# Optimization experiments

Hardware: AMD Instinct MI355X
Metric: run time of the kernel (lower is better)

The kernel has to match this reference:

```python
import jax, jax.numpy as jnp
import numpy as np

N, E, EMB, H, DH, FF, L = 2500, 10000, 32, 4, 8, 32, 1
EPS = 1e-5


def setup_inputs() -> dict:
    key = jax.random.key(0)
    ks = jax.random.split(key, 20)
    rn = lambda k, shape, s=0.1: jax.random.normal(k, shape, jnp.float32) * s
    return {
        'feat': rn(ks[0], (N, EMB), 1.0),
        'query': rn(ks[1], (E, L, H, DH)),
        'src_key_w': rn(ks[2], (E, L, H, FF, EMB)),
        'dst_key_w': rn(ks[3], (E, L, H, FF, EMB)),
        'src_key_b': rn(ks[4], (E, L, H, FF)),
        'dst_key_b': rn(ks[5], (E, L, H, FF)),
        'edge_key_w': rn(ks[6], (E, L, H, FF, DH)),
        'edge_key_b': rn(ks[7], (E, L, H, DH)),
        'src_val_w': rn(ks[8], (E, L, H, FF, EMB)),
        'dst_val_w': rn(ks[9], (E, L, H, FF, EMB)),
        'src_val_b': rn(ks[10], (E, L, H, FF)),
        'dst_val_b': rn(ks[11], (E, L, H, FF)),
        'edge_val_w': rn(ks[12], (E, L, H, FF, DH)),
        'edge_val_b': rn(ks[13], (E, L, H, DH)),
        'key_gamma': jnp.ones((DH,), jnp.float32),
        'key_beta': jnp.zeros((DH,), jnp.float32),
        'val_gamma': jnp.ones((DH,), jnp.float32),
        'val_beta': jnp.zeros((DH,), jnp.float32),
        'out_gamma': jnp.ones((DH,), jnp.float32),
        'out_beta': jnp.zeros((DH,), jnp.float32),
        'src': jax.random.randint(ks[14], (E,), 0, N, jnp.int32),
        'dst': jax.random.randint(ks[15], (E,), 0, N, jnp.int32),
        'i': 0,
    }


def _ln(x, g, b):
    m = x.mean(-1, keepdims=True)
    v = x.var(-1, keepdims=True)
    return (x - m) * jax.lax.rsqrt(v + EPS) * g + b


def _ffn(fs, fd, uw, vw, ub, vb, ew, eb, g, b):
    # per-edge, per-head two-layer feedforward with distinct weights
    # fs, fd: (E, EMB); uw/vw: (E,H,FF,EMB); ew: (E,H,FF,DH)
    h = (jnp.einsum('ehfd,ed->ehf', uw, fs) + ub
         + jnp.einsum('ehfd,ed->ehf', vw, fd) + vb)
    h = jax.nn.relu(h)
    o = jnp.einsum('ehfk,ehf->ehk', ew, h) + eb  # (E,H,DH)
    return _ln(o, g, b)


def reference(feat, query, src_key_w, dst_key_w, src_key_b, dst_key_b,
              edge_key_w, edge_key_b, src_val_w, dst_val_w, src_val_b,
              dst_val_b, edge_val_w, edge_val_b, key_gamma, key_beta,
              val_gamma, val_beta, out_gamma, out_beta, src, dst, i):
    n = feat.shape[0]
    fs, fd = feat[src], feat[dst]
    k = _ffn(fs, fd, src_key_w[:, i], dst_key_w[:, i], src_key_b[:, i],
             dst_key_b[:, i], edge_key_w[:, i], edge_key_b[:, i],
             key_gamma, key_beta)
    logits = (k * query[:, i]).sum(-1)  # (E,H)
    # edge softmax grouped by destination node
    m = jax.ops.segment_max(logits, dst, num_segments=n)
    ex = jnp.exp(logits - m[dst])
    s = jax.ops.segment_sum(ex, dst, num_segments=n)
    attn = ex / s[dst]  # (E,H)
    v = _ffn(fs, fd, src_val_w[:, i], dst_val_w[:, i], src_val_b[:, i],
             dst_val_b[:, i], edge_val_w[:, i], edge_val_b[:, i],
             val_gamma, val_beta)
    msg = v * attn[..., None]  # (E,H,DH)
    agg = jax.ops.segment_sum(msg, dst, num_segments=n)  # (N,H,DH)
    out = _ln(agg, out_gamma, out_beta)
    return out.reshape(feat.shape), attn
```

## Files before the change

kernel.cpp:

```cpp
#include <hip/hip_runtime.h>

#define NN   2500
#define NE   10000
#define EMBD 32
#define NH   4
#define DHD  8
#define FFD  32
#define EPSC 1e-5f

typedef float vf4 __attribute__((ext_vector_type(4)));

__device__ __forceinline__ float dot4v(vf4 a, vf4 b) {
    return a.x * b.x + a.y * b.y + a.z * b.z + a.w * b.w;
}

__device__ __forceinline__ vf4 ffn_compute(
    const vf4* U, const vf4* V, vf4 E, vf4 FS, vf4 FD,
    float b1, vf4 b2, vf4 g4, vf4 bt4, int lane)
{
    float p0 = dot4v(U[0], FS) + dot4v(V[0], FD);
    float p1 = dot4v(U[1], FS) + dot4v(V[1], FD);
    float p2 = dot4v(U[2], FS) + dot4v(V[2], FD);
    float p3 = dot4v(U[3], FS) + dot4v(V[3], FD);
    #pragma unroll
    for (int m = 1; m <= 4; m <<= 1) {
        p0 += __shfl_xor(p0, m); p1 += __shfl_xor(p1, m);
        p2 += __shfl_xor(p2, m); p3 += __shfl_xor(p3, m);
    }

    int f = lane >> 1;
    int s = ((f & 7) << 3) | (lane & 7);
    float h0 = __shfl(p0, s), h1 = __shfl(p1, s);
    float h2 = __shfl(p2, s), h3 = __shfl(p3, s);
    int j = lane >> 4;
    float hp = (j == 0) ? h0 : (j == 1) ? h1 : (j == 2) ? h2 : h3;
    float h  = fmaxf(hp + b1, 0.0f);

    vf4 o = E * h;
    #pragma unroll
    for (int m = 2; m <= 32; m <<= 1) {
        o.x += __shfl_xor(o.x, m); o.y += __shfl_xor(o.y, m);
        o.z += __shfl_xor(o.z, m); o.w += __shfl_xor(o.w, m);
    }
    o += b2;

    float s1 = o.x + o.y + o.z + o.w;
    float s2 = o.x * o.x + o.y * o.y + o.z * o.z + o.w * o.w;
    s1 += __shfl_xor(s1, 1);
    s2 += __shfl_xor(s2, 1);
    float mean = s1 * 0.125f;
    float var  = s2 * 0.125f - mean * mean;
    float rs   = rsqrtf(var + EPSC);
    return (o - mean) * rs * g4 + bt4;
}

__global__ void edge_kernel(
    const float* __restrict__ feat, const float* __restrict__ query,
    const float* __restrict__ skw, const float* __restrict__ dkw,
    const float* __restrict__ skb, const float* __restrict__ dkb,
    const float* __restrict__ ekw, const float* __restrict__ ekb,
    const float* __restrict__ svw, const float* __restrict__ dvw,
    const float* __restrict__ svb, const float* __restrict__ dvb,
    const float* __restrict__ evw, const float* __restrict__ evb,
    const float* __restrict__ kg, const float* __restrict__ kbeta,
    const float* __restrict__ vg, const float* __restrict__ vbeta,
    const int* __restrict__ src, const int* __restrict__ dst,
    float* __restrict__ s_den, float* __restrict__ ex_out,
    float* __restrict__ v_out)
{
    int gid = blockIdx.x * 256 + threadIdx.x;
    int wid = gid >> 6;
    if (wid >= NE * NH) return;
    int lane = threadIdx.x & 63;
    int e    = wid >> 2;
    int hh   = wid & 3;
    int c    = lane & 7;
    int f    = lane >> 1;
    int half = lane & 1;
    int sn = src[e], dn = dst[e];
    size_t eh = (size_t)wid;

    const vf4* ku_p = (const vf4*)(skw + eh * 1024);
    const vf4* kv_p = (const vf4*)(dkw + eh * 1024);
    const vf4* vu_p = (const vf4*)(svw + eh * 1024);
    const vf4* vv_p = (const vf4*)(dvw + eh * 1024);
    vf4 KU[4], KV[4], VU[4], VV[4];
    #pragma unroll
    for (int j = 0; j < 4; j++) KU[j] = ku_p[j * 64 + lane];
    #pragma unroll
    for (int j = 0; j < 4; j++) KV[j] = kv_p[j * 64 + lane];
    #pragma unroll
    for (int j = 0; j < 4; j++) VU[j] = vu_p[j * 64 + lane];
    #pragma unroll
    for (int j = 0; j < 4; j++) VV[j] = vv_p[j * 64 + lane];
    vf4 KE = ((const vf4*)(ekw + eh * 256))[lane];
    vf4 VE = ((const vf4*)(evw + eh * 256))[lane];
    vf4 FS = ((const vf4*)(feat + sn * EMBD))[c];
    vf4 FD = ((const vf4*)(feat + dn * EMBD))[c];
    vf4 q4 = ((const vf4*)(query + eh * 8))[half];

    float kb1 = skb[eh * 32 + f] + dkb[eh * 32 + f];
    float vb1 = svb[eh * 32 + f] + dvb[eh * 32 + f];
    vf4 kb2 = ((const vf4*)(ekb + eh * 8))[half];
    vf4 vb2 = ((const vf4*)(evb + eh * 8))[half];
    vf4 kgam = ((const vf4*)kg)[half],   kbet = ((const vf4*)kbeta)[half];
    vf4 vgam = ((const vf4*)vg)[half],   vbet = ((const vf4*)vbeta)[half];

    vf4 kn = ffn_compute(KU, KV, KE, FS, FD, kb1, kb2, kgam, kbet, lane);
    float lp = dot4v(kn, q4);
    lp += __shfl_xor(lp, 1);

    vf4 vn = ffn_compute(VU, VV, VE, FS, FD, vb1, vb2, vgam, vbet, lane);

    if (lane < 2)
        *(vf4*)(v_out + eh * 8 + half * 4) = vn;
    if (lane == 0) {
        float exv = expf(lp);
        ex_out[eh] = exv;
        atomicAdd(s_den + dn * NH + hh, exv);
    }
}

__global__ void zero_kernel(float* __restrict__ p, int n) {
    int i = blockIdx.x * blockDim.x + threadIdx.x;
    if (i < n) p[i] = 0.0f;
}

__global__ void attn_agg_kernel(
    const int* __restrict__ dst, const float* __restrict__ ex,
    const float* __restrict__ s_den, const float* __restrict__ v,
    float* __restrict__ agg, float* __restrict__ attn_out)
{
    int tid = blockIdx.x * blockDim.x + threadIdx.x;
    if (tid >= NE * NH * DHD) return;
    int eh = tid >> 3;
    int dd = tid & 7;
    int e  = eh >> 2;
    int h  = eh & 3;
    int dn = dst[e];
    float a = ex[eh] / s_den[dn * NH + h];
    if (dd == 0) attn_out[eh] = a;
    atomicAdd(agg + (dn * NH + h) * DHD + dd, v[tid] * a);
}

__global__ void out_ln_kernel(
    const float* __restrict__ agg, const float* __restrict__ g,
    const float* __restrict__ b, float* __restrict__ out)
{
    int tid = blockIdx.x * blockDim.x + threadIdx.x;
    if (tid >= NN * NH) return;
    vf4 a0 = *(const vf4*)(agg + tid * 8);
    vf4 a1 = *(const vf4*)(agg + tid * 8 + 4);
    float s1 = a0.x + a0.y + a0.z + a0.w + a1.x + a1.y + a1.z + a1.w;
    float s2 = a0.x * a0.x + a0.y * a0.y + a0.z * a0.z + a0.w * a0.w
             + a1.x * a1.x + a1.y * a1.y + a1.z * a1.z + a1.w * a1.w;
    float mean = s1 * 0.125f;
    float var  = s2 * 0.125f - mean * mean;
    float rs   = rsqrtf(var + EPSC);
    vf4 g0 = *(const vf4*)(g);
    vf4 g1 = *(const vf4*)(g + 4);
    vf4 b0 = *(const vf4*)(b);
    vf4 b1 = *(const vf4*)(b + 4);
    *(vf4*)(out + tid * 8)     = (a0 - mean) * rs * g0 + b0;
    *(vf4*)(out + tid * 8 + 4) = (a1 - mean) * rs * g1 + b1;
}

extern "C" void kernel_launch(void* const* d_in, const int* in_sizes, int n_in,
                              void* d_out, int out_size, void* d_ws, size_t ws_size,
                              hipStream_t stream) {
    const float* feat  = (const float*)d_in[0];
    const float* query = (const float*)d_in[1];
    const float* skw   = (const float*)d_in[2];
    const float* dkw   = (const float*)d_in[3];
    const float* skb   = (const float*)d_in[4];
    const float* dkb   = (const float*)d_in[5];
    const float* ekw   = (const float*)d_in[6];
    const float* ekb   = (const float*)d_in[7];
    const float* svw   = (const float*)d_in[8];
    const float* dvw   = (const float*)d_in[9];
    const float* svb   = (const float*)d_in[10];
    const float* dvb   = (const float*)d_in[11];
    const float* evw   = (const float*)d_in[12];
    const float* evb   = (const float*)d_in[13];
    const float* kg    = (const float*)d_in[14];
    const float* kbeta = (const float*)d_in[15];
    const float* vg    = (const float*)d_in[16];
    const float* vbeta = (const float*)d_in[17];
    const float* og    = (const float*)d_in[18];
    const float* obeta = (const float*)d_in[19];
    const int*   src   = (const int*)d_in[20];
    const int*   dst   = (const int*)d_in[21];

    float* ws    = (float*)d_ws;
    float* s_den = ws;
    float* agg   = ws + 10000;
    float* ex    = ws + 90000;
    float* vbuf  = ws + 130000;

    float* out  = (float*)d_out;

    zero_kernel<<<(90000 + 255) / 256, 256, 0, stream>>>(ws, 90000);

    edge_kernel<<<(NE * NH * 64) / 256, 256, 0, stream>>>(
        feat, query, skw, dkw, skb, dkb, ekw, ekb,
        svw, dvw, svb, dvb, evw, evb,
        kg, kbeta, vg, vbeta, src, dst,
        s_den, ex, vbuf);

    attn_agg_kernel<<<(NE * NH * DHD + 255) / 256, 256, 0, stream>>>(
        dst, ex, s_den, vbuf, agg, out + NN * EMBD);

    out_ln_kernel<<<(NN * NH + 255) / 256, 256, 0, stream>>>(
        agg, og, obeta, out);
}
```

Baseline: 143.5 us.

## Fuse attention aggregation into edge kernel, normalize by denominator in final pass

The edge kernel now atomically accumulates exp(logit)*v directly into the per-node aggregate, and a single final kernel divides by the softmax denominator before the output layernorm and also writes the attention weights. This removes the separate v buffer round-trip and one kernel launch. The zero kernel is replaced with hipMemsetAsync, and the streamed weight loads are marked nontemporal to avoid cache pollution. The unnormalized exp without max subtraction is kept as before, with some overflow risk, and the atomic count per edge-head stays the same.

```diff
diff --git a/kernel.cpp b/kernel.cpp
--- a/kernel.cpp
+++ b/kernel.cpp
@@ -27,7 +27,6 @@
         p0 += __shfl_xor(p0, m); p1 += __shfl_xor(p1, m);
         p2 += __shfl_xor(p2, m); p3 += __shfl_xor(p3, m);
     }
-
     int f = lane >> 1;
     int s = ((f & 7) << 3) | (lane & 7);
     float h0 = __shfl(p0, s), h1 = __shfl(p1, s);
@@ -65,8 +64,8 @@
     const float* __restrict__ kg, const float* __restrict__ kbeta,
     const float* __restrict__ vg, const float* __restrict__ vbeta,
     const int* __restrict__ src, const int* __restrict__ dst,
-    float* __restrict__ s_den, float* __restrict__ ex_out,
-    float* __restrict__ v_out)
+    float* __restrict__ s_den, float* __restrict__ agg,
+    float* __restrict__ ex_out)
 {
     int gid = blockIdx.x * 256 + threadIdx.x;
     int wid = gid >> 6;
@@ -86,23 +85,25 @@
     const vf4* vv_p = (const vf4*)(dvw + eh * 1024);
     vf4 KU[4], KV[4], VU[4], VV[4];
     #pragma unroll
-    for (int j = 0; j < 4; j++) KU[j] = ku_p[j * 64 + lane];
-    #pragma unroll
-    for (int j = 0; j < 4; j++) KV[j] = kv_p[j * 64 + lane];
-    #pragma unroll
-    for (int j = 0; j < 4; j++) VU[j] = vu_p[j * 64 + lane];
-    #pragma unroll
-    for (int j = 0; j < 4; j++) VV[j] = vv_p[j * 64 + lane];
-    vf4 KE = ((const vf4*)(ekw + eh * 256))[lane];
-    vf4 VE = ((const vf4*)(evw + eh * 256))[lane];
+    for (int j = 0; j < 4; j++) KU[j] = __builtin_nontemporal_load(&ku_p[j * 64 + lane]);
+    #pragma unroll
+    for (int j = 0; j < 4; j++) KV[j] = __builtin_nontemporal_load(&kv_p[j * 64 + lane]);
+    #pragma unroll
+    for (int j = 0; j < 4; j++) VU[j] = __builtin_nontemporal_load(&vu_p[j * 64 + lane]);
+    #pragma unroll
+    for (int j = 0; j < 4; j++) VV[j] = __builtin_nontemporal_load(&vv_p[j * 64 + lane]);
+    vf4 KE = __builtin_nontemporal_load(&((const vf4*)(ekw + eh * 256))[lane]);
+    vf4 VE = __builtin_nontemporal_load(&((const vf4*)(evw + eh * 256))[lane]);
     vf4 FS = ((const vf4*)(feat + sn * EMBD))[c];
     vf4 FD = ((const vf4*)(feat + dn * EMBD))[c];
-    vf4 q4 = ((const vf4*)(query + eh * 8))[half];
-
-    float kb1 = skb[eh * 32 + f] + dkb[eh * 32 + f];
-    float vb1 = svb[eh * 32 + f] + dvb[eh * 32 + f];
-    vf4 kb2 = ((const vf4*)(ekb + eh * 8))[half];
-    vf4 vb2 = ((const vf4*)(evb + eh * 8))[half];
+    vf4 q4 = __builtin_nontemporal_load(&((const vf4*)(query + eh * 8))[half]);
+
+    float kb1 = __builtin_nontemporal_load(skb + eh * 32 + f)
+              + __builtin_nontemporal_load(dkb + eh * 32 + f);
+    float vb1 = __builtin_nontemporal_load(svb + eh * 32 + f)
+              + __builtin_nontemporal_load(dvb + eh * 32 + f);
+    vf4 kb2 = __builtin_nontemporal_load(&((const vf4*)(ekb + eh * 8))[half]);
+    vf4 vb2 = __builtin_nontemporal_load(&((const vf4*)(evb + eh * 8))[half]);
     vf4 kgam = ((const vf4*)kg)[half],   kbet = ((const vf4*)kbeta)[half];
     vf4 vgam = ((const vf4*)vg)[half],   vbet = ((const vf4*)vbeta)[half];
 
@@ -112,57 +113,49 @@
 
     vf4 vn = ffn_compute(VU, VV, VE, FS, FD, vb1, vb2, vgam, vbet, lane);
 
-    if (lane < 2)
-        *(vf4*)(v_out + eh * 8 + half * 4) = vn;
+    float exv = expf(lp);
+    if (lane < 2) {
+        float* ap = agg + ((size_t)dn * NH + hh) * DHD + half * 4;
+        atomicAdd(ap + 0, exv * vn.x);
+        atomicAdd(ap + 1, exv * vn.y);
+        atomicAdd(ap + 2, exv * vn.z);
+        atomicAdd(ap + 3, exv * vn.w);
+    }
     if (lane == 0) {
-        float exv = expf(lp);
         ex_out[eh] = exv;
         atomicAdd(s_den + dn * NH + hh, exv);
     }
 }
 
-__global__ void zero_kernel(float* __restrict__ p, int n) {
-    int i = blockIdx.x * blockDim.x + threadIdx.x;
-    if (i < n) p[i] = 0.0f;
-}
-
-__global__ void attn_agg_kernel(
+__global__ void final_kernel(
     const int* __restrict__ dst, const float* __restrict__ ex,
-    const float* __restrict__ s_den, const float* __restrict__ v,
-    float* __restrict__ agg, float* __restrict__ attn_out)
+    const float* __restrict__ s_den, const float* __restrict__ agg,
+    const float* __restrict__ g, const float* __restrict__ b,
+    float* __restrict__ out, float* __restrict__ attn_out)
 {
     int tid = blockIdx.x * blockDim.x + threadIdx.x;
-    if (tid >= NE * NH * DHD) return;
-    int eh = tid >> 3;
-    int dd = tid & 7;
-    int e  = eh >> 2;
-    int h  = eh & 3;
-    int dn = dst[e];
-    float a = ex[eh] / s_den[dn * NH + h];
-    if (dd == 0) attn_out[eh] = a;
-    atomicAdd(agg + (dn * NH + h) * DHD + dd, v[tid] * a);
-}
-
-__global__ void out_ln_kernel(
-    const float* __restrict__ agg, const float* __restrict__ g,
-    const float* __restrict__ b, float* __restrict__ out)
-{
-    int tid = blockIdx.x * blockDim.x + threadIdx.x;
-    if (tid >= NN * NH) return;
-    vf4 a0 = *(const vf4*)(agg + tid * 8);
-    vf4 a1 = *(const vf4*)(agg + tid * 8 + 4);
-    float s1 = a0.x + a0.y + a0.z + a0.w + a1.x + a1.y + a1.z + a1.w;
-    float s2 = a0.x * a0.x + a0.y * a0.y + a0.z * a0.z + a0.w * a0.w
-             + a1.x * a1.x + a1.y * a1.y + a1.z * a1.z + a1.w * a1.w;
-    float mean = s1 * 0.125f;
-    float var  = s2 * 0.125f - mean * mean;
-    float rs   = rsqrtf(var + EPSC);
-    vf4 g0 = *(const vf4*)(g);
-    vf4 g1 = *(const vf4*)(g + 4);
-    vf4 b0 = *(const vf4*)(b);
-    vf4 b1 = *(const vf4*)(b + 4);
-    *(vf4*)(out + tid * 8)     = (a0 - mean) * rs * g0 + b0;
-    *(vf4*)(out + tid * 8 + 4) = (a1 - mean) * rs * g1 + b1;
+    if (tid < NE * NH) {
+        int e = tid >> 2, h = tid & 3;
+        attn_out[tid] = ex[tid] / s_den[dst[e] * NH + h];
+    } else if (tid < NE * NH + NN * NH) {
+        int t = tid - NE * NH;
+        float s = s_den[t];
+        float inv = (s > 0.0f) ? 1.0f / s : 0.0f;
+        vf4 a0 = *(const vf4*)(agg + t * 8)     * inv;
+        vf4 a1 = *(const vf4*)(agg + t * 8 + 4) * inv;
+        float s1 = a0.x + a0.y + a0.z + a0.w + a1.x + a1.y + a1.z + a1.w;
+        float s2 = a0.x * a0.x + a0.y * a0.y + a0.z * a0.z + a0.w * a0.w
+                 + a1.x * a1.x + a1.y * a1.y + a1.z * a1.z + a1.w * a1.w;
+        float mean = s1 * 0.125f;
+        float var  = s2 * 0.125f - mean * mean;
+        float rs   = rsqrtf(var + EPSC);
+        vf4 g0 = *(const vf4*)(g);
+        vf4 g1 = *(const vf4*)(g + 4);
+        vf4 b0 = *(const vf4*)(b);
+        vf4 b1 = *(const vf4*)(b + 4);
+        *(vf4*)(out + t * 8)     = (a0 - mean) * rs * g0 + b0;
+        *(vf4*)(out + t * 8 + 4) = (a1 - mean) * rs * g1 + b1;
+    }
 }
 
 extern "C" void kernel_launch(void* const* d_in, const int* in_sizes, int n_in,
@@ -195,21 +188,17 @@
     float* s_den = ws;
     float* agg   = ws + 10000;
     float* ex    = ws + 90000;
-    float* vbuf  = ws + 130000;
 
     float* out  = (float*)d_out;
 
-    zero_kernel<<<(90000 + 255) / 256, 256, 0, stream>>>(ws, 90000);
+    hipMemsetAsync(ws, 0, 90000 * sizeof(float), stream);
 
     edge_kernel<<<(NE * NH * 64) / 256, 256, 0, stream>>>(
         feat, query, skw, dkw, skb, dkb, ekw, ekb,
         svw, dvw, svb, dvb, evw, evb,
         kg, kbeta, vg, vbeta, src, dst,
-        s_den, ex, vbuf);
-
-    attn_agg_kernel<<<(NE * NH * DHD + 255) / 256, 256, 0, stream>>>(
-        dst, ex, s_den, vbuf, agg, out + NN * EMBD);
-
-    out_ln_kernel<<<(NN * NH + 255) / 256, 256, 0, stream>>>(
-        agg, og, obeta, out);
-}
+        s_den, agg, ex);
+
+    final_kernel<<<(NE * NH + NN * NH + 255) / 256, 256, 0, stream>>>(
+        dst, ex, s_den, agg, og, obeta, out, out + NN * EMBD);
+}
```

New measurement: 127.2 us. 11.3% less time.
